# Optimization experiments

Hardware: AMD Instinct MI355X
Metric: run time of the kernel (lower is better)

The kernel has to match this reference:

```python
import jax, jax.numpy as jnp
import numpy as np

BLANK = 0          # tf.nn.ctc_loss default blank_index (StringLookup reserves 0 for OOV)
PAD = 127          # padding_value = char_to_num.vocabulary_size()
NEG = -1e30        # log-space 'zero' (avoid -inf to keep grads NaN-free)
B, T, C, L = 1024, 256, 128, 32


def setup_inputs() -> dict:
    key = jax.random.key(0)
    k1, k2 = jax.random.split(key)
    # labels in [1, PAD-1]; none equal PAD so label_length == L (full-length labels)
    y_true = jax.random.randint(k1, (B, L), 1, PAD).astype(jnp.int32)
    y_pred = jax.random.normal(k2, (B, T, C), dtype=jnp.float32)
    return {"y_true": y_true, "y_pred": y_pred}


def _ctc_loss(y_true, y_pred):
    """Faithful jax version of tf.nn.ctc_loss(labels, logits, label_len, T,
    logits_time_major=False, blank_index=0): standard log-space alpha DP."""
    Bn, Tn, Cn = y_pred.shape
    Ln = y_true.shape[1]
    S = 2 * Ln + 1  # extended label length (blanks interleaved)

    logp = jax.nn.log_softmax(y_pred, axis=-1)                    # [B,T,C]

    # extended label sequence: blank, l1, blank, l2, ..., blank   # [B,S]
    ext = jnp.full((Bn, S), BLANK, dtype=y_true.dtype)
    ext = ext.at[:, 1::2].set(y_true)

    # log-probs gathered at extended-label symbols                # [B,T,S]
    lp_ext = jnp.take_along_axis(
        logp, jnp.broadcast_to(ext[:, None, :], (Bn, Tn, S)), axis=2)

    # label_length = count of non-padding entries (mirrors count_nonzero)
    label_len = jnp.sum(y_true != PAD, axis=1)                    # [B]

    # skip transition s-2 -> s allowed iff ext[s] is a non-blank differing
    # from ext[s-2]
    skip_ok = jnp.concatenate(
        [jnp.zeros((Bn, 2), bool),
         (ext[:, 2:] != BLANK) & (ext[:, 2:] != ext[:, :-2])], axis=1)  # [B,S]

    neg1 = jnp.full((Bn, 1), NEG, logp.dtype)
    neg2 = jnp.full((Bn, 2), NEG, logp.dtype)

    alpha0 = jnp.full((Bn, S), NEG, logp.dtype)
    alpha0 = alpha0.at[:, 0].set(lp_ext[:, 0, 0]).at[:, 1].set(lp_ext[:, 0, 1])

    def step(alpha, lp_t):  # alpha,[B,S]  lp_t,[B,S]
        a1 = jnp.concatenate([neg1, alpha[:, :-1]], axis=1)
        a2 = jnp.concatenate([neg2, alpha[:, :-2]], axis=1)
        a2 = jnp.where(skip_ok, a2, NEG)
        new = lp_t + jnp.logaddexp(jnp.logaddexp(alpha, a1), a2)
        return new, None

    lp_seq = jnp.transpose(lp_ext, (1, 0, 2))                     # [T,B,S]
    alphaT, _ = jax.lax.scan(step, alpha0, lp_seq[1:])            # [B,S]

    # total log-likelihood ends at last blank (2*len) or last label (2*len-1)
    bi = jnp.arange(Bn)
    e1 = 2 * label_len
    e2 = 2 * label_len - 1
    loglik = jnp.logaddexp(alphaT[bi, e1], alphaT[bi, e2])        # [B]
    return -loglik


def reference(y_true, y_pred):
    # The original layer returns y_pred and registers the loss via add_loss;
    # the compute-dominant quantity is the per-example CTC loss, returned here.
    return _ctc_loss(y_true, y_pred)
```

## Files before the change

### kernel.cpp

```cpp
#include <hip/hip_runtime.h>
#include <cstdint>


#define CTC_BLANK 0
#define CTC_PAD   127
#define NEG       (-1e30f)
#define LOG2E     1.44269504088896340736f
#define LN2       0.69314718055994530942f

constexpr int Bn = 1024, Tn = 256, Cn = 128, Ln = 32;
constexpr int NSLOT = Ln + 1;
constexpr int NCH = 2;
constexpr int CR  = Tn / NCH;

__device__ __forceinline__ float fexp2(float x) { return __builtin_amdgcn_exp2f(x); }
__device__ __forceinline__ float flog2(float x) { return __builtin_amdgcn_logf(x); }

template <int CTRL>
__device__ __forceinline__ float dpp_add(float s) {
    int v = __builtin_amdgcn_update_dpp(0, __float_as_int(s), CTRL, 0xF, 0xF, true);
    return s + __int_as_float(v);
}
__device__ __forceinline__ float dpp_wave_shr1(float src, float old) {
    return __int_as_float(__builtin_amdgcn_update_dpp(
        __float_as_int(old), __float_as_int(src), 0x138, 0xF, 0xF, false));
}

__global__ __launch_bounds__(512, 8) void ctc_fused_kernel(
        const int*   __restrict__ y_true,
        const float* __restrict__ y_pred,
        float*       __restrict__ out)
{
    __shared__ _Float16 Gc[Tn * NSLOT];
    __shared__ int   labels[Ln];
    __shared__ __align__(16) int cmap[Cn];
    __shared__ int   used[Cn];
    __shared__ int   wcnt[8];
    __shared__ float partS[16];

    const int b    = blockIdx.x;
    const int tid  = threadIdx.x;
    const int lane = tid & 63;
    const int wave = tid >> 6;

    if (tid < Ln) labels[tid] = y_true[b * Ln + tid];
    if (tid < Cn) used[tid] = 0;
    __syncthreads();
    if (tid == 0) used[CTC_BLANK] = 1;
    if (tid < Ln) used[labels[tid]] = 1;
    __syncthreads();
    {
        bool f = (tid < Cn) && (used[tid] != 0);
        unsigned long long m = __ballot(f);
        if (lane == 0) wcnt[wave] = __popcll(m);
        __syncthreads();
        int base = 0;
        for (int w = 0; w < wave; ++w) base += wcnt[w];
        if (tid < Cn)
            cmap[tid] = f ? (base + __popcll(m & ((1ull << lane) - 1ull))) : -1;
        __syncthreads();
    }

    const float* rowbase = y_pred + (size_t)b * Tn * Cn;
    const int half = lane >> 5;
    const int l32  = lane & 31;
    const int4 cm  = ((const int4*)cmap)[l32];
    float acc = 0.f;

    const int  i      = lane;
    const bool validO = (i < Ln);
    const bool validE = (i <= Ln);
    const int  myLab   = validO ? labels[i] : -1;
    const int  prevLab = (i >= 1 && i < Ln) ? labels[i - 1] : -1;
    const int  slotO   = validO ? cmap[myLab] : 0;
    const bool skipO   = (i >= 1 && i < Ln) &&
                         (myLab != CTC_BLANK) && (myLab != prevLab);
    const int  len = __popcll(__ballot(validO && (myLab != CTC_PAD)));
    float aE = NEG, aO = NEG;

    auto dp_chunk = [&](int t0, int t1) {
        int t = t0;
        if (t == 0) {
            aE = (i == 0) ? (float)Gc[0]     : NEG;
            aO = (i == 0) ? (float)Gc[slotO] : NEG;
            t = 1;
        }
        float pB[2], pO[2];
        const int ta = t, tb = (t + 1 < t1) ? t + 1 : t1 - 1;
        pB[0] = (float)Gc[ta * NSLOT]; pO[0] = (float)Gc[ta * NSLOT + slotO];
        pB[1] = (float)Gc[tb * NSLOT]; pO[1] = (float)Gc[tb * NSLOT + slotO];
        int k = 0;
        #pragma unroll 2
        for (; t < t1; ++t) {
            const float lpB = pB[k], lpO = pO[k];
            const int tp = (t + 2 < t1) ? t + 2 : t1 - 1;
            pB[k] = (float)Gc[tp * NSLOT];
            pO[k] = (float)Gc[tp * NSLOT + slotO];
            k ^= 1;

            const float aOup = dpp_wave_shr1(aO, NEG);
            const float m  = fmaxf(aE, aOup);
            const float e1 = fexp2(aE - m);
            const float e2 = fexp2(aOup - m);
            const float sE = e1 + e2;
            const float nE = lpB + m + flog2(sE);
            const float m3 = fmaxf(aO, m);
            const float nO = lpO + m3 +
                flog2(fexp2(aO - m3) + (skipO ? sE : e1) * fexp2(m - m3));
            aE = validE ? nE : NEG;
            aO = validO ? nO : NEG;
        }
    };

    for (int c = 0; c < NCH; ++c) {
        if (wave == 0 && c > 0) dp_chunk((c - 1) * CR, c * CR);

        const int cbase = c * CR;
        float4 v[8];
        #pragma unroll
        for (int j = 0; j < 8; ++j) {
            const int r = cbase + 2 * (wave * 8 + j) + half;
            v[j] = ((const float4*)(rowbase + r * Cn))[l32];
        }
        #pragma unroll
        for (int j = 0; j < 8; ++j) {
            const int r = cbase + 2 * (wave * 8 + j) + half;
            const float4 x = v[j];
            if (cm.x >= 0) Gc[r * NSLOT + cm.x] = (_Float16)(x.x * LOG2E);
            if (cm.y >= 0) Gc[r * NSLOT + cm.y] = (_Float16)(x.y * LOG2E);
            if (cm.z >= 0) Gc[r * NSLOT + cm.z] = (_Float16)(x.z * LOG2E);
            if (cm.w >= 0) Gc[r * NSLOT + cm.w] = (_Float16)(x.w * LOG2E);
            float s = __expf(x.x) + __expf(x.y) + __expf(x.z) + __expf(x.w);
            s = dpp_add<0x111>(s);
            s = dpp_add<0x112>(s);
            s = dpp_add<0x114>(s);
            s = dpp_add<0x118>(s);
            s = dpp_add<0x142>(s);
            acc += __logf(s);
        }
        if (c == NCH - 1 && l32 == 31) partS[wave * 2 + half] = acc;
        __syncthreads();
    }

    if (wave == 0) {
        dp_chunk((NCH - 1) * CR, Tn);
        const float v1 = __shfl(aE, len, 64);
        const float v2 = __shfl(aO, len - 1, 64);
        if (i == 0) {
            float S = 0.f;
            #pragma unroll
            for (int j = 0; j < 16; ++j) S += partS[j];
            const float mm = fmaxf(v1, v2);
            const float L2 = mm + flog2(fexp2(v1 - mm) + fexp2(v2 - mm));
            out[b] = S - LN2 * L2;
        }
    }
}

extern "C" void kernel_launch(void* const* d_in, const int* in_sizes, int n_in,
                              void* d_out, int out_size, void* d_ws, size_t ws_size,
                              hipStream_t stream) {
    const int*   y_true = (const int*)d_in[0];
    const float* y_pred = (const float*)d_in[1];
    float*       out    = (float*)d_out;
    ctc_fused_kernel<<<Bn, 512, 0, stream>>>(y_true, y_pred, out);
}
```

Baseline: 209.3 us.

## Double-buffer logit chunks into LDS via async global_load_lds

Splits the time axis into 16-row chunks and stages each chunk into a double-buffered LDS area with global_load_lds, issuing the next chunk's copy before converting the current one. Wave 0 runs the alpha recursion for the previous chunk after its own conversion, so the serial DP is spread over many short barrier intervals while loads are in flight. The aim is to hide global load latency behind conversion and DP work. In exchange it adds 16 KB of LDS per block, which may lower occupancy, and many more block-wide barriers that force all waves to wait on wave 0's DP each chunk.

Measured after the change: 206.7 us. Within noise of the previous version (-1.2%).

```diff
diff --git a/kernel.cpp b/kernel.cpp
--- a/kernel.cpp
+++ b/kernel.cpp
@@ -10,8 +10,9 @@
 
 constexpr int Bn = 1024, Tn = 256, Cn = 128, Ln = 32;
 constexpr int NSLOT = Ln + 1;
-constexpr int NCH = 2;
-constexpr int CR  = Tn / NCH;
+constexpr int CR  = 16;
+constexpr int NCH = Tn / CR;
+constexpr int CF  = CR * Cn;
 
 __device__ __forceinline__ float fexp2(float x) { return __builtin_amdgcn_exp2f(x); }
 __device__ __forceinline__ float flog2(float x) { return __builtin_amdgcn_logf(x); }
@@ -25,12 +26,18 @@
     return __int_as_float(__builtin_amdgcn_update_dpp(
         __float_as_int(old), __float_as_int(src), 0x138, 0xF, 0xF, false));
 }
+__device__ __forceinline__ void gl_lds16(const float* g, float* l) {
+    __builtin_amdgcn_global_load_lds(
+        (const __attribute__((address_space(1))) uint32_t*)g,
+        (__attribute__((address_space(3))) uint32_t*)l, 16, 0, 0);
+}
 
 __global__ __launch_bounds__(512, 8) void ctc_fused_kernel(
         const int*   __restrict__ y_true,
         const float* __restrict__ y_pred,
         float*       __restrict__ out)
 {
+    __shared__ __align__(16) float raw[2][CF];
     __shared__ _Float16 Gc[Tn * NSLOT];
     __shared__ int   labels[Ln];
     __shared__ __align__(16) int cmap[Cn];
@@ -42,6 +49,14 @@
     const int tid  = threadIdx.x;
     const int lane = tid & 63;
     const int wave = tid >> 6;
+
+    const float* gbase = y_pred + (size_t)b * Tn * Cn;
+
+    auto stage = [&](int c, int buf) {
+        gl_lds16(gbase + c * CF + tid * 4, &raw[buf][wave * 256]);
+    };
+
+    stage(0, 0);
 
     if (tid < Ln) labels[tid] = y_true[b * Ln + tid];
     if (tid < Cn) used[tid] = 0;
@@ -61,7 +76,6 @@
         __syncthreads();
     }
 
-    const float* rowbase = y_pred + (size_t)b * Tn * Cn;
     const int half = lane >> 5;
     const int l32  = lane & 31;
     const int4 cm  = ((const int4*)cmap)[l32];
@@ -113,19 +127,12 @@
     };
 
     for (int c = 0; c < NCH; ++c) {
-        if (wave == 0 && c > 0) dp_chunk((c - 1) * CR, c * CR);
+        if (c + 1 < NCH) stage(c + 1, (c + 1) & 1);
 
-        const int cbase = c * CR;
-        float4 v[8];
-        #pragma unroll
-        for (int j = 0; j < 8; ++j) {
-            const int r = cbase + 2 * (wave * 8 + j) + half;
-            v[j] = ((const float4*)(rowbase + r * Cn))[l32];
-        }
-        #pragma unroll
-        for (int j = 0; j < 8; ++j) {
-            const int r = cbase + 2 * (wave * 8 + j) + half;
-            const float4 x = v[j];
+        {
+            const int rl = 2 * wave + half;
+            const int r  = c * CR + rl;
+            const float4 x = ((const float4*)&raw[c & 1][rl * Cn])[l32];
             if (cm.x >= 0) Gc[r * NSLOT + cm.x] = (_Float16)(x.x * LOG2E);
             if (cm.y >= 0) Gc[r * NSLOT + cm.y] = (_Float16)(x.y * LOG2E);
             if (cm.z >= 0) Gc[r * NSLOT + cm.z] = (_Float16)(x.z * LOG2E);
@@ -138,12 +145,14 @@
             s = dpp_add<0x142>(s);
             acc += __logf(s);
         }
+
+        if (wave == 0 && c > 0) dp_chunk((c - 1) * CR, c * CR);
         if (c == NCH - 1 && l32 == 31) partS[wave * 2 + half] = acc;
         __syncthreads();
     }
 
     if (wave == 0) {
-        dp_chunk((NCH - 1) * CR, Tn);
+        dp_chunk(Tn - CR, Tn);
         const float v1 = __shfl(aE, len, 64);
         const float v2 = __shfl(aO, len - 1, 64);
         if (i == 0) {
```
